# Performance work log

Hardware: AMD Instinct MI355X
Metric: run time of the kernel (lower is better)

The kernel has to match this reference:

```python
import jax, jax.numpy as jnp
import numpy as np

N = 100000      # nodes
E = 1600000     # edges
G = 1024        # graphs in batch
BASE = 1000     # baseline (TF-IDF) dim
AUG = 384       # augmented (LM) dim
H = 256         # hidden dim
C = 2           # classes
EPS = 1e-5      # BatchNorm eps


def setup_inputs() -> dict:
    key = jax.random.key(0)
    ks = jax.random.split(key, 10)
    x = jax.random.normal(ks[0], (N, BASE), jnp.float32)
    x_aug = jax.random.normal(ks[1], (N, AUG), jnp.float32)
    edge_index = jax.random.randint(ks[2], (2, E), 0, N)
    batch = jnp.sort(jax.random.randint(ks[3], (N,), 0, G))

    def lin(k, fin, fout):
        return (jax.random.normal(k, (fin, fout), jnp.float32) / np.sqrt(fin)).astype(jnp.float32)

    return dict(
        x=x, x_aug=x_aug,
        fusion_W=lin(ks[4], BASE + AUG, H), fusion_b=jnp.zeros((H,), jnp.float32),
        W0=lin(ks[5], H, H), b0=jnp.zeros((H,), jnp.float32),
        g0=jnp.ones((H,), jnp.float32), be0=jnp.zeros((H,), jnp.float32),
        W1=lin(ks[6], H, H), b1=jnp.zeros((H,), jnp.float32),
        g1=jnp.ones((H,), jnp.float32), be1=jnp.zeros((H,), jnp.float32),
        fc_W=lin(ks[7], H, C), fc_b=jnp.zeros((C,), jnp.float32),
        edge_index=edge_index, batch=batch,
    )


def _gcn(h, W, b, src, dst, dinv):
    # PyG GCNConv: x' = D^{-1/2}(A+I)D^{-1/2} (x W) + b, self-loop weight 1
    h = h @ W                                     # [N, H]
    norm = dinv[src] * dinv[dst]                  # [E]
    agg = jax.ops.segment_sum(h[src] * norm[:, None], dst, num_segments=N)
    agg = agg + h * (dinv * dinv)[:, None]        # self-loop term
    return agg + b


def _bn(x, gamma, beta):
    # training-mode BatchNorm1d (batch statistics, biased variance)
    m = x.mean(axis=0)
    v = x.var(axis=0)
    return (x - m) * jax.lax.rsqrt(v + EPS) * gamma + beta


def reference(x, x_aug, fusion_W, fusion_b, W0, b0, g0, be0, W1, b1, g1, be1,
              fc_W, fc_b, edge_index, batch):
    src, dst = edge_index[0], edge_index[1]
    # degrees with self-loops (edge weight 1), scattered at destination
    deg = jnp.zeros((N,), x.dtype).at[dst].add(1.0) + 1.0
    dinv = jax.lax.rsqrt(deg)

    # feature fusion ('concat'): Linear(baseline+aug -> hidden) + ReLU
    h = jax.nn.relu(jnp.concatenate([x, x_aug], axis=1) @ fusion_W + fusion_b)

    # GCN layer 1 + BN + ReLU (dropout is identity in eval)
    h = jax.nn.relu(_bn(_gcn(h, W0, b0, src, dst, dinv), g0, be0))
    # GCN layer 2 + BN + ReLU
    h = jax.nn.relu(_bn(_gcn(h, W1, b1, src, dst, dinv), g1, be1))

    # global mean pool over graphs
    cnt = jax.ops.segment_sum(jnp.ones((N,), h.dtype), batch, num_segments=G)
    pooled = jax.ops.segment_sum(h, batch, num_segments=G) / jnp.maximum(cnt, 1.0)[:, None]

    logits = pooled @ fc_W + fc_b                 # [G, C]
    return jax.nn.log_softmax(logits, axis=1)
```

## Files before the change

### kernel.cpp

```cpp
#include <hip/hip_runtime.h>
#include <hip/hip_bf16.h>

#define N_NODES 100000
#define N_EDGES 1600000
#define N_GRAPH 1024
#define DIM_BASE 1000
#define DIM_AUG 384
#define DIM_IN 1384
#define KPAD_IN 1408
#define HD 256
#define BN_EPS 1e-5f

typedef _Float16 f16x8 __attribute__((ext_vector_type(8)));
typedef _Float16 f16x4 __attribute__((ext_vector_type(4)));
typedef float f32x4 __attribute__((ext_vector_type(4)));

__global__ void zero_kernel(unsigned int* __restrict__ p, int n) {
    int i = blockIdx.x * blockDim.x + threadIdx.x;
    if (i < n) p[i] = 0u;
}

__global__ void count_edges_kernel(const int* __restrict__ dst, int* __restrict__ counts, int e) {
    int i = blockIdx.x * blockDim.x + threadIdx.x;
    if (i < e) atomicAdd(&counts[dst[i]], 1);
}

__global__ __launch_bounds__(256) void deg_bsum_kernel(const int* __restrict__ counts,
                                                       int* __restrict__ bsum, int n) {
    __shared__ int sh[256];
    int t = threadIdx.x;
    int base = blockIdx.x * 1024 + t * 4;
    int s = 0;
    if (base < n) {
        int4 v = *(const int4*)&counts[base];
        s = v.x + v.y + v.z + v.w;
    }
    sh[t] = s;
    __syncthreads();
    for (int off = 128; off > 0; off >>= 1) {
        if (t < off) sh[t] += sh[t + off];
        __syncthreads();
    }
    if (t == 0) bsum[blockIdx.x] = sh[0];
}

__global__ __launch_bounds__(128) void scan_bsum_kernel(const int* __restrict__ bsum,
                                                        int* __restrict__ boff, int nb) {
    __shared__ int sh[128];
    int t = threadIdx.x;
    int v = (t < nb) ? bsum[t] : 0;
    sh[t] = v;
    __syncthreads();
    for (int off = 1; off < 128; off <<= 1) {
        int u = (t >= off) ? sh[t - off] : 0;
        __syncthreads();
        sh[t] += u;
        __syncthreads();
    }
    if (t < nb) boff[t] = sh[t] - v;
}

__global__ __launch_bounds__(256) void emit_csr_kernel(const int* __restrict__ counts,
                                                       const int* __restrict__ boff,
                                                       int* __restrict__ row_ptr,
                                                       int* __restrict__ cursor,
                                                       float* __restrict__ dinv, int n, int etot) {
    __shared__ int sh[256];
    int t = threadIdx.x;
    int base = blockIdx.x * 1024 + t * 4;
    int c0 = 0, c1 = 0, c2 = 0, c3 = 0;
    if (base < n) {
        int4 v = *(const int4*)&counts[base];
        c0 = v.x; c1 = v.y; c2 = v.z; c3 = v.w;
    }
    int s = c0 + c1 + c2 + c3;
    sh[t] = s;
    __syncthreads();
    for (int off = 1; off < 256; off <<= 1) {
        int u = (t >= off) ? sh[t - off] : 0;
        __syncthreads();
        sh[t] += u;
        __syncthreads();
    }
    if (base < n) {
        int run = boff[blockIdx.x] + sh[t] - s;
        int4 rp;
        rp.x = run; run += c0;
        rp.y = run; run += c1;
        rp.z = run; run += c2;
        rp.w = run;
        *(int4*)&row_ptr[base] = rp;
        *(int4*)&cursor[base] = rp;
        float4 dv;
        dv.x = rsqrtf((float)c0 + 1.0f);
        dv.y = rsqrtf((float)c1 + 1.0f);
        dv.z = rsqrtf((float)c2 + 1.0f);
        dv.w = rsqrtf((float)c3 + 1.0f);
        *(float4*)&dinv[base] = dv;
    }
    if (blockIdx.x == 0 && t == 0) row_ptr[n] = etot;
}

__global__ void fill_edges_kernel(const int* __restrict__ src, const int* __restrict__ dst,
                                  int* __restrict__ cursor, int* __restrict__ col, int e) {
    int i = blockIdx.x * blockDim.x + threadIdx.x;
    if (i < e) {
        int pos = atomicAdd(&cursor[dst[i]], 1);
        col[pos] = src[i];
    }
}

__global__ __launch_bounds__(256) void btrans_kernel(const float* __restrict__ W,
                                                     f16x8* __restrict__ Bt,
                                                     int K, int nchunks) {
    int idx = blockIdx.x * 256 + threadIdx.x;
    if (idx >= nchunks) return;
    int col = idx & 255;
    int kbase = (idx >> 8) * 8;
    f16x8 h;
#pragma unroll
    for (int j = 0; j < 8; ++j) {
        int k = kbase + j;
        float v = (k < K) ? W[(size_t)k * HD + col] : 0.f;
        h[j] = (_Float16)v;
    }
    Bt[idx] = h;
}

__global__ __launch_bounds__(512, 4) void fusion_mfma_kernel(
        const float* __restrict__ x, const float* __restrict__ xa,
        const f16x8* __restrict__ Bt, const float* __restrict__ bias,
        _Float16* __restrict__ C, int M) {
    __shared__ _Float16 Al[128 * 40];
    __shared__ _Float16 Bl[32 * 256];
    int tid = threadIdx.x;
    int lane = tid & 63;
    int wid = tid >> 6;
    int wr = wid >> 2, wc = wid & 3;
    int l16 = lane & 15, l4 = lane >> 4;
    int row0 = blockIdx.x * 128;

    f32x4 acc[4][4];
#pragma unroll
    for (int m = 0; m < 4; ++m)
#pragma unroll
        for (int n = 0; n < 4; ++n) acc[m][n] = (f32x4){0.f, 0.f, 0.f, 0.f};

    int arow = tid >> 2;
    int akq = (tid & 3) * 8;
    int ar = row0 + arow;

    const int S = KPAD_IN / 32;
    for (int s = 0; s < S; ++s) {
        int kg = s * 32 + akq;
        float fv[8];
#pragma unroll
        for (int j = 0; j < 8; ++j) fv[j] = 0.f;
        if (ar < M && kg < DIM_IN) {
            const float* sp = (kg < DIM_BASE) ? (x + (size_t)ar * DIM_BASE + kg)
                                              : (xa + (size_t)ar * DIM_AUG + (kg - DIM_BASE));
            float4 v0 = ((const float4*)sp)[0];
            float4 v1 = ((const float4*)sp)[1];
            fv[0] = v0.x; fv[1] = v0.y; fv[2] = v0.z; fv[3] = v0.w;
            fv[4] = v1.x; fv[5] = v1.y; fv[6] = v1.z; fv[7] = v1.w;
        }
        f16x8 av;
#pragma unroll
        for (int j = 0; j < 8; ++j) av[j] = (_Float16)fv[j];
        f16x8 bv0 = Bt[(size_t)s * 1024 + tid];
        f16x8 bv1 = Bt[(size_t)s * 1024 + 512 + tid];

        __syncthreads();
        *(f16x8*)&Al[arow * 40 + akq] = av;
        *(f16x8*)&Bl[(size_t)tid * 8] = bv0;
        *(f16x8*)&Bl[(size_t)(512 + tid) * 8] = bv1;
        __syncthreads();

        f16x8 bf[4];
#pragma unroll
        for (int n = 0; n < 4; ++n)
            bf[n] = *(const f16x8*)&Bl[(size_t)(l4 * 256 + wc * 64 + n * 16 + l16) * 8];
#pragma unroll
        for (int m = 0; m < 4; ++m) {
            f16x8 af = *(const f16x8*)&Al[(size_t)(wr * 64 + m * 16 + l16) * 40 + l4 * 8];
#pragma unroll
            for (int n = 0; n < 4; ++n)
                acc[m][n] = __builtin_amdgcn_mfma_f32_16x16x32_f16(af, bf[n], acc[m][n], 0, 0, 0);
        }
    }

#pragma unroll
    for (int n = 0; n < 4; ++n) {
        int colF = wc * 64 + n * 16 + l16;
        float bcol = bias[colF];
#pragma unroll
        for (int m = 0; m < 4; ++m) {
#pragma unroll
            for (int r = 0; r < 4; ++r) {
                int rowF = row0 + wr * 64 + m * 16 + l4 * 4 + r;
                if (rowF < M)
                    C[(size_t)rowF * HD + colF] = (_Float16)fmaxf(acc[m][n][r] + bcol, 0.f);
            }
        }
    }
}

__global__ __launch_bounds__(512, 4) void hgemm_f16_kernel(
        const _Float16* __restrict__ A, const f16x8* __restrict__ Bt,
        _Float16* __restrict__ C, int M) {
    __shared__ _Float16 Al[128 * 40];
    __shared__ _Float16 Bl[32 * 256];
    int tid = threadIdx.x;
    int lane = tid & 63;
    int wid = tid >> 6;
    int wr = wid >> 2, wc = wid & 3;
    int l16 = lane & 15, l4 = lane >> 4;
    int row0 = blockIdx.x * 128;

    f32x4 acc[4][4];
#pragma unroll
    for (int m = 0; m < 4; ++m)
#pragma unroll
        for (int n = 0; n < 4; ++n) acc[m][n] = (f32x4){0.f, 0.f, 0.f, 0.f};

    int arow = tid >> 2;
    int akq = (tid & 3) * 8;
    int ar = row0 + arow;

    const int S = HD / 32;
    for (int s = 0; s < S; ++s) {
        int kg = s * 32 + akq;
        f16x8 av = (f16x8)(_Float16)0;
        if (ar < M) av = *(const f16x8*)&A[(size_t)ar * HD + kg];
        f16x8 bv0 = Bt[(size_t)s * 1024 + tid];
        f16x8 bv1 = Bt[(size_t)s * 1024 + 512 + tid];

        __syncthreads();
        *(f16x8*)&Al[arow * 40 + akq] = av;
        *(f16x8*)&Bl[(size_t)tid * 8] = bv0;
        *(f16x8*)&Bl[(size_t)(512 + tid) * 8] = bv1;
        __syncthreads();

        f16x8 bf[4];
#pragma unroll
        for (int n = 0; n < 4; ++n)
            bf[n] = *(const f16x8*)&Bl[(size_t)(l4 * 256 + wc * 64 + n * 16 + l16) * 8];
#pragma unroll
        for (int m = 0; m < 4; ++m) {
            f16x8 af = *(const f16x8*)&Al[(size_t)(wr * 64 + m * 16 + l16) * 40 + l4 * 8];
#pragma unroll
            for (int n = 0; n < 4; ++n)
                acc[m][n] = __builtin_amdgcn_mfma_f32_16x16x32_f16(af, bf[n], acc[m][n], 0, 0, 0);
        }
    }

#pragma unroll
    for (int n = 0; n < 4; ++n) {
        int colF = wc * 64 + n * 16 + l16;
#pragma unroll
        for (int m = 0; m < 4; ++m) {
#pragma unroll
            for (int r = 0; r < 4; ++r) {
                int rowF = row0 + wr * 64 + m * 16 + l4 * 4 + r;
                if (rowF < M)
                    C[(size_t)rowF * HD + colF] = (_Float16)acc[m][n][r];
            }
        }
    }
}

__global__ __launch_bounds__(512, 4) void hgemm_bn_kernel(
        const float* __restrict__ A, const f16x8* __restrict__ Bt,
        const float* __restrict__ bnp, _Float16* __restrict__ C, int M) {
    __shared__ _Float16 Al[128 * 40];
    __shared__ _Float16 Bl[32 * 256];
    __shared__ float bns[512];
    int tid = threadIdx.x;
    int lane = tid & 63;
    int wid = tid >> 6;
    int wr = wid >> 2, wc = wid & 3;
    int l16 = lane & 15, l4 = lane >> 4;
    int row0 = blockIdx.x * 128;

    bns[tid] = bnp[tid & 511];

    f32x4 acc[4][4];
#pragma unroll
    for (int m = 0; m < 4; ++m)
#pragma unroll
        for (int n = 0; n < 4; ++n) acc[m][n] = (f32x4){0.f, 0.f, 0.f, 0.f};

    int arow = tid >> 2;
    int akq = (tid & 3) * 8;
    int ar = row0 + arow;

    __syncthreads();

    const int S = HD / 32;
    for (int s = 0; s < S; ++s) {
        int kg = s * 32 + akq;
        float fv[8];
#pragma unroll
        for (int j = 0; j < 8; ++j) fv[j] = 0.f;
        if (ar < M) {
            const float* sp = A + (size_t)ar * HD + kg;
            float4 v0 = ((const float4*)sp)[0];
            float4 v1 = ((const float4*)sp)[1];
            fv[0] = v0.x; fv[1] = v0.y; fv[2] = v0.z; fv[3] = v0.w;
            fv[4] = v1.x; fv[5] = v1.y; fv[6] = v1.z; fv[7] = v1.w;
        }
        f16x8 av;
#pragma unroll
        for (int j = 0; j < 8; ++j)
            av[j] = (_Float16)fmaxf(fmaf(fv[j], bns[kg + j], bns[HD + kg + j]), 0.f);
        f16x8 bv0 = Bt[(size_t)s * 1024 + tid];
        f16x8 bv1 = Bt[(size_t)s * 1024 + 512 + tid];

        __syncthreads();
        *(f16x8*)&Al[arow * 40 + akq] = av;
        *(f16x8*)&Bl[(size_t)tid * 8] = bv0;
        *(f16x8*)&Bl[(size_t)(512 + tid) * 8] = bv1;
        __syncthreads();

        f16x8 bf[4];
#pragma unroll
        for (int n = 0; n < 4; ++n)
            bf[n] = *(const f16x8*)&Bl[(size_t)(l4 * 256 + wc * 64 + n * 16 + l16) * 8];
#pragma unroll
        for (int m = 0; m < 4; ++m) {
            f16x8 af = *(const f16x8*)&Al[(size_t)(wr * 64 + m * 16 + l16) * 40 + l4 * 8];
#pragma unroll
            for (int n = 0; n < 4; ++n)
                acc[m][n] = __builtin_amdgcn_mfma_f32_16x16x32_f16(af, bf[n], acc[m][n], 0, 0, 0);
        }
    }

#pragma unroll
    for (int n = 0; n < 4; ++n) {
        int colF = wc * 64 + n * 16 + l16;
#pragma unroll
        for (int m = 0; m < 4; ++m) {
#pragma unroll
            for (int r = 0; r < 4; ++r) {
                int rowF = row0 + wr * 64 + m * 16 + l4 * 4 + r;
                if (rowF < M)
                    C[(size_t)rowF * HD + colF] = (_Float16)acc[m][n][r];
            }
        }
    }
}

__global__ __launch_bounds__(256) void agg_kernel(
        const _Float16* __restrict__ t, const float* __restrict__ dinv,
        const int* __restrict__ row_ptr, const int* __restrict__ col,
        const float* __restrict__ bias, float* __restrict__ outp, int n) {
    int wid = threadIdx.x >> 6;
    int lane = threadIdx.x & 63;
    int i = blockIdx.x * 4 + wid;
    if (i >= n) return;
    int c0 = lane * 4;
    float di = dinv[i];
    float di2 = di * di;
    f16x4 sv = *(const f16x4*)&t[(size_t)i * HD + c0];
    float a0 = (float)sv[0] * di2, a1 = (float)sv[1] * di2;
    float a2 = (float)sv[2] * di2, a3 = (float)sv[3] * di2;
    int e = row_ptr[i], end = row_ptr[i + 1];
    for (; e + 1 < end; e += 2) {
        int s0 = col[e], s1 = col[e + 1];
        float w0 = dinv[s0] * di, w1 = dinv[s1] * di;
        f16x4 v0 = *(const f16x4*)&t[(size_t)s0 * HD + c0];
        f16x4 v1 = *(const f16x4*)&t[(size_t)s1 * HD + c0];
        a0 = fmaf((float)v0[0], w0, a0); a1 = fmaf((float)v0[1], w0, a1);
        a2 = fmaf((float)v0[2], w0, a2); a3 = fmaf((float)v0[3], w0, a3);
        a0 = fmaf((float)v1[0], w1, a0); a1 = fmaf((float)v1[1], w1, a1);
        a2 = fmaf((float)v1[2], w1, a2); a3 = fmaf((float)v1[3], w1, a3);
    }
    if (e < end) {
        int s0 = col[e];
        float w0 = dinv[s0] * di;
        f16x4 v0 = *(const f16x4*)&t[(size_t)s0 * HD + c0];
        a0 = fmaf((float)v0[0], w0, a0); a1 = fmaf((float)v0[1], w0, a1);
        a2 = fmaf((float)v0[2], w0, a2); a3 = fmaf((float)v0[3], w0, a3);
    }
    float4 b = *(const float4*)&bias[c0];
    float4 o;
    o.x = a0 + b.x; o.y = a1 + b.y; o.z = a2 + b.z; o.w = a3 + b.w;
    *(float4*)&outp[(size_t)i * HD + c0] = o;
}

__global__ __launch_bounds__(256) void bn_stats_kernel(const float* __restrict__ a,
                                                       float* __restrict__ sums, int n) {
    int tid = threadIdx.x;
    int r0 = blockIdx.x * 256;
    int r1 = min(r0 + 256, n);
    float s = 0.f, s2 = 0.f;
    for (int r = r0; r < r1; ++r) {
        float v = a[(size_t)r * HD + tid];
        s += v;
        s2 = fmaf(v, v, s2);
    }
    atomicAdd(&sums[tid], s);
    atomicAdd(&sums[HD + tid], s2);
}

__global__ __launch_bounds__(256) void bn_final_kernel(const float* __restrict__ sums,
                                                       const float* __restrict__ g,
                                                       const float* __restrict__ be,
                                                       float* __restrict__ p, int n) {
    int tid = threadIdx.x;
    float mean = sums[tid] / (float)n;
    float var = sums[HD + tid] / (float)n - mean * mean;
    float sc = g[tid] * rsqrtf(var + BN_EPS);
    p[tid] = sc;
    p[HD + tid] = be[tid] - mean * sc;
}

__global__ void graph_cnt_kernel(const int* __restrict__ batch, float* __restrict__ cnt, int n) {
    int i = blockIdx.x * blockDim.x + threadIdx.x;
    if (i < n) atomicAdd(&cnt[batch[i]], 1.0f);
}

__global__ __launch_bounds__(256) void bn_relu_pool_kernel(const float* __restrict__ a,
                                                           const float* __restrict__ p,
                                                           const int* __restrict__ batch,
                                                           float* __restrict__ pooled, int n) {
    int tid = threadIdx.x;
    int n0 = blockIdx.x * 64;
    int n1 = min(n0 + 64, n);
    if (n0 >= n) return;
    float sc = p[tid], sh = p[HD + tid];
    int curg = batch[n0];
    float acc = 0.f;
    for (int i = n0; i < n1; ++i) {
        int g = batch[i];
        if (g != curg) {
            atomicAdd(&pooled[(size_t)curg * HD + tid], acc);
            acc = 0.f;
            curg = g;
        }
        acc += fmaxf(fmaf(a[(size_t)i * HD + tid], sc, sh), 0.f);
    }
    atomicAdd(&pooled[(size_t)curg * HD + tid], acc);
}

__global__ __launch_bounds__(64) void head_kernel(const float* __restrict__ pooled,
                                                  const float* __restrict__ cnt,
                                                  const float* __restrict__ fcW,
                                                  const float* __restrict__ fcb,
                                                  float* __restrict__ outp) {
    int g = blockIdx.x, lane = threadIdx.x;
    float inv = 1.0f / fmaxf(cnt[g], 1.0f);
    float a0 = 0.f, a1 = 0.f;
    for (int j = lane; j < HD; j += 64) {
        float v = pooled[(size_t)g * HD + j] * inv;
        a0 = fmaf(v, fcW[j * 2 + 0], a0);
        a1 = fmaf(v, fcW[j * 2 + 1], a1);
    }
    for (int off = 32; off > 0; off >>= 1) {
        a0 += __shfl_down(a0, off);
        a1 += __shfl_down(a1, off);
    }
    if (lane == 0) {
        float l0 = a0 + fcb[0], l1 = a1 + fcb[1];
        float m = fmaxf(l0, l1);
        float lse = m + logf(expf(l0 - m) + expf(l1 - m));
        outp[g * 2 + 0] = l0 - lse;
        outp[g * 2 + 1] = l1 - lse;
    }
}

extern "C" void kernel_launch(void* const* d_in, const int* in_sizes, int n_in,
                              void* d_out, int out_size, void* d_ws, size_t ws_size,
                              hipStream_t stream) {
    const float* x        = (const float*)d_in[0];
    const float* x_aug    = (const float*)d_in[1];
    const float* fusion_W = (const float*)d_in[2];
    const float* fusion_b = (const float*)d_in[3];
    const float* W0       = (const float*)d_in[4];
    const float* b0       = (const float*)d_in[5];
    const float* g0       = (const float*)d_in[6];
    const float* be0      = (const float*)d_in[7];
    const float* W1       = (const float*)d_in[8];
    const float* b1       = (const float*)d_in[9];
    const float* g1       = (const float*)d_in[10];
    const float* be1      = (const float*)d_in[11];
    const float* fc_W     = (const float*)d_in[12];
    const float* fc_b     = (const float*)d_in[13];
    const int*   eidx     = (const int*)d_in[14];
    const int*   batch    = (const int*)d_in[15];
    float* outp = (float*)d_out;

    const int N = N_NODES, E = N_EDGES, G = N_GRAPH;
    const int* src = eidx;
    const int* dst = eidx + E;

    size_t off = 0;
    char* ws = (char*)d_ws;
    auto take = [&](size_t nbytes) -> void* {
        void* p = ws + off;
        off = (off + nbytes + 255) & ~(size_t)255;
        return p;
    };
    float*     bufA    = (float*)take((size_t)N * HD * 4);
    _Float16*  bufH    = (_Float16*)take((size_t)N * HD * 2);
    _Float16*  bufT    = (_Float16*)take((size_t)N * HD * 2);
    float*     dinv    = (float*)take((size_t)N * 4);
    int*       row_ptr = (int*)take((size_t)(N + 1) * 4);
    int*       cursor  = (int*)take((size_t)N * 4);
    int*       col     = (int*)take((size_t)E * 4);
    float*     bn1p    = (float*)take(512 * 4);
    float*     bn2p    = (float*)take(512 * 4);
    int*       bsum    = (int*)take(128 * 4);
    int*       boff    = (int*)take(128 * 4);
    f16x8*     BtF     = (f16x8*)take((size_t)(KPAD_IN / 8) * 256 * 16);
    f16x8*     Bt0     = (f16x8*)take((size_t)(HD / 8) * 256 * 16);
    f16x8*     Bt1     = (f16x8*)take((size_t)(HD / 8) * 256 * 16);
    size_t zwords = (size_t)N + 512 + 512 + (size_t)G * HD + G;
    unsigned int* zbase = (unsigned int*)take(zwords * 4);
    int*   counts = (int*)zbase;
    float* bn1s   = (float*)(zbase + N);
    float* bn2s   = bn1s + 512;
    float* pooled = bn2s + 512;
    float* cnt    = pooled + (size_t)G * HD;

    const int nchF = (KPAD_IN / 8) * 256;
    const int nchH = (HD / 8) * 256;
    const int nScanB = (N + 1023) / 1024;

    zero_kernel<<<(int)((zwords + 255) / 256), 256, 0, stream>>>(zbase, (int)zwords);
    count_edges_kernel<<<(E + 255) / 256, 256, 0, stream>>>(dst, counts, E);
    deg_bsum_kernel<<<nScanB, 256, 0, stream>>>(counts, bsum, N);
    scan_bsum_kernel<<<1, 128, 0, stream>>>(bsum, boff, nScanB);
    emit_csr_kernel<<<nScanB, 256, 0, stream>>>(counts, boff, row_ptr, cursor, dinv, N, E);
    fill_edges_kernel<<<(E + 255) / 256, 256, 0, stream>>>(src, dst, cursor, col, E);
    btrans_kernel<<<(nchF + 255) / 256, 256, 0, stream>>>(fusion_W, BtF, DIM_IN, nchF);
    btrans_kernel<<<(nchH + 255) / 256, 256, 0, stream>>>(W0, Bt0, HD, nchH);
    btrans_kernel<<<(nchH + 255) / 256, 256, 0, stream>>>(W1, Bt1, HD, nchH);

    const int gblocks = (N + 127) / 128;
    fusion_mfma_kernel<<<gblocks, 512, 0, stream>>>(x, x_aug, BtF, fusion_b, bufH, N);
    hgemm_f16_kernel<<<gblocks, 512, 0, stream>>>(bufH, Bt0, bufT, N);
    agg_kernel<<<(N + 3) / 4, 256, 0, stream>>>(bufT, dinv, row_ptr, col, b0, bufA, N);
    bn_stats_kernel<<<(N + 255) / 256, 256, 0, stream>>>(bufA, bn1s, N);
    bn_final_kernel<<<1, 256, 0, stream>>>(bn1s, g0, be0, bn1p, N);
    hgemm_bn_kernel<<<gblocks, 512, 0, stream>>>(bufA, Bt1, bn1p, bufT, N);
    agg_kernel<<<(N + 3) / 4, 256, 0, stream>>>(bufT, dinv, row_ptr, col, b1, bufA, N);
    bn_stats_kernel<<<(N + 255) / 256, 256, 0, stream>>>(bufA, bn2s, N);
    bn_final_kernel<<<1, 256, 0, stream>>>(bn2s, g1, be1, bn2p, N);
    graph_cnt_kernel<<<(N + 255) / 256, 256, 0, stream>>>(batch, cnt, N);
    bn_relu_pool_kernel<<<(N + 63) / 64, 256, 0, stream>>>(bufA, bn2p, batch, pooled, N);
    head_kernel<<<G, 64, 0, stream>>>(pooled, cnt, fc_W, fc_b, outp);
}
```

Measured before the change: 1.002 ms.

## Double-buffer A tiles in LDS, prefetch A two steps ahead, read B from global

All three GEMM kernels now double-buffer the A tile in shared memory with one barrier per k-step instead of two. A-tile global loads are issued two steps ahead into registers so they overlap the MFMA work. The B operand no longer goes through LDS; each wave reads its B fragments straight from global memory (likely L2/L1 hits) into registers. Out-of-range rows are clamped instead of branched on. This cuts barrier and LDS traffic at the cost of more global B reads and register pressure.

```diff
diff --git a/kernel.cpp b/kernel.cpp
--- a/kernel.cpp
+++ b/kernel.cpp
@@ -131,8 +131,7 @@
         const float* __restrict__ x, const float* __restrict__ xa,
         const f16x8* __restrict__ Bt, const float* __restrict__ bias,
         _Float16* __restrict__ C, int M) {
-    __shared__ _Float16 Al[128 * 40];
-    __shared__ _Float16 Bl[32 * 256];
+    __shared__ _Float16 Al[2][128 * 40];
     int tid = threadIdx.x;
     int lane = tid & 63;
     int wid = tid >> 6;
@@ -149,57 +148,67 @@
     int arow = tid >> 2;
     int akq = (tid & 3) * 8;
     int ar = row0 + arow;
-
-    const int S = KPAD_IN / 32;
-    for (int s = 0; s < S; ++s) {
+    int arc = (ar < M) ? ar : (M - 1);
+
+    auto loadA = [&](int s, float* fv) {
         int kg = s * 32 + akq;
-        float fv[8];
-#pragma unroll
-        for (int j = 0; j < 8; ++j) fv[j] = 0.f;
-        if (ar < M && kg < DIM_IN) {
-            const float* sp = (kg < DIM_BASE) ? (x + (size_t)ar * DIM_BASE + kg)
-                                              : (xa + (size_t)ar * DIM_AUG + (kg - DIM_BASE));
+        if (kg < DIM_IN) {
+            const float* sp = (kg < DIM_BASE) ? (x + (size_t)arc * DIM_BASE + kg)
+                                              : (xa + (size_t)arc * DIM_AUG + (kg - DIM_BASE));
             float4 v0 = ((const float4*)sp)[0];
             float4 v1 = ((const float4*)sp)[1];
             fv[0] = v0.x; fv[1] = v0.y; fv[2] = v0.z; fv[3] = v0.w;
             fv[4] = v1.x; fv[5] = v1.y; fv[6] = v1.z; fv[7] = v1.w;
-        }
+        } else {
+#pragma unroll
+            for (int j = 0; j < 8; ++j) fv[j] = 0.f;
+        }
+    };
+
+    const int S = KPAD_IN / 32;
+    float fv0[8], fv1[8];
+    loadA(0, fv0);
+    loadA(1, fv1);
+
+    int bcol = wc * 64 + l16;
+
+    auto iter = [&](int s, float* fv) {
+        int buf = s & 1;
         f16x8 av;
 #pragma unroll
         for (int j = 0; j < 8; ++j) av[j] = (_Float16)fv[j];
-        f16x8 bv0 = Bt[(size_t)s * 1024 + tid];
-        f16x8 bv1 = Bt[(size_t)s * 1024 + 512 + tid];
-
-        __syncthreads();
-        *(f16x8*)&Al[arow * 40 + akq] = av;
-        *(f16x8*)&Bl[(size_t)tid * 8] = bv0;
-        *(f16x8*)&Bl[(size_t)(512 + tid) * 8] = bv1;
-        __syncthreads();
-
+        *(f16x8*)&Al[buf][arow * 40 + akq] = av;
+        if (s + 2 < S) loadA(s + 2, fv);
+        __syncthreads();
         f16x8 bf[4];
 #pragma unroll
         for (int n = 0; n < 4; ++n)
-            bf[n] = *(const f16x8*)&Bl[(size_t)(l4 * 256 + wc * 64 + n * 16 + l16) * 8];
+            bf[n] = Bt[(size_t)(s * 4 + l4) * 256 + bcol + n * 16];
 #pragma unroll
         for (int m = 0; m < 4; ++m) {
-            f16x8 af = *(const f16x8*)&Al[(size_t)(wr * 64 + m * 16 + l16) * 40 + l4 * 8];
+            f16x8 af = *(const f16x8*)&Al[buf][(wr * 64 + m * 16 + l16) * 40 + l4 * 8];
 #pragma unroll
             for (int n = 0; n < 4; ++n)
                 acc[m][n] = __builtin_amdgcn_mfma_f32_16x16x32_f16(af, bf[n], acc[m][n], 0, 0, 0);
         }
+    };
+
+    for (int s = 0; s < S; s += 2) {
+        iter(s, fv0);
+        iter(s + 1, fv1);
     }
 
 #pragma unroll
     for (int n = 0; n < 4; ++n) {
         int colF = wc * 64 + n * 16 + l16;
-        float bcol = bias[colF];
+        float bc = bias[colF];
 #pragma unroll
         for (int m = 0; m < 4; ++m) {
 #pragma unroll
             for (int r = 0; r < 4; ++r) {
                 int rowF = row0 + wr * 64 + m * 16 + l4 * 4 + r;
                 if (rowF < M)
-                    C[(size_t)rowF * HD + colF] = (_Float16)fmaxf(acc[m][n][r] + bcol, 0.f);
+                    C[(size_t)rowF * HD + colF] = (_Float16)fmaxf(acc[m][n][r] + bc, 0.f);
             }
         }
     }
@@ -208,8 +217,7 @@
 __global__ __launch_bounds__(512, 4) void hgemm_f16_kernel(
         const _Float16* __restrict__ A, const f16x8* __restrict__ Bt,
         _Float16* __restrict__ C, int M) {
-    __shared__ _Float16 Al[128 * 40];
-    __shared__ _Float16 Bl[32 * 256];
+    __shared__ _Float16 Al[2][128 * 40];
     int tid = threadIdx.x;
     int lane = tid & 63;
     int wid = tid >> 6;
@@ -226,32 +234,34 @@
     int arow = tid >> 2;
     int akq = (tid & 3) * 8;
     int ar = row0 + arow;
+    int arc = (ar < M) ? ar : (M - 1);
+    int bcol = wc * 64 + l16;
 
     const int S = HD / 32;
-    for (int s = 0; s < S; ++s) {
-        int kg = s * 32 + akq;
-        f16x8 av = (f16x8)(_Float16)0;
-        if (ar < M) av = *(const f16x8*)&A[(size_t)ar * HD + kg];
-        f16x8 bv0 = Bt[(size_t)s * 1024 + tid];
-        f16x8 bv1 = Bt[(size_t)s * 1024 + 512 + tid];
-
-        __syncthreads();
-        *(f16x8*)&Al[arow * 40 + akq] = av;
-        *(f16x8*)&Bl[(size_t)tid * 8] = bv0;
-        *(f16x8*)&Bl[(size_t)(512 + tid) * 8] = bv1;
-        __syncthreads();
-
+    f16x8 av0 = *(const f16x8*)&A[(size_t)arc * HD + akq];
+    f16x8 av1 = *(const f16x8*)&A[(size_t)arc * HD + 32 + akq];
+
+    auto iter = [&](int s, f16x8& av) {
+        int buf = s & 1;
+        *(f16x8*)&Al[buf][arow * 40 + akq] = av;
+        if (s + 2 < S) av = *(const f16x8*)&A[(size_t)arc * HD + (s + 2) * 32 + akq];
+        __syncthreads();
         f16x8 bf[4];
 #pragma unroll
         for (int n = 0; n < 4; ++n)
-            bf[n] = *(const f16x8*)&Bl[(size_t)(l4 * 256 + wc * 64 + n * 16 + l16) * 8];
+            bf[n] = Bt[(size_t)(s * 4 + l4) * 256 + bcol + n * 16];
 #pragma unroll
         for (int m = 0; m < 4; ++m) {
-            f16x8 af = *(const f16x8*)&Al[(size_t)(wr * 64 + m * 16 + l16) * 40 + l4 * 8];
+            f16x8 af = *(const f16x8*)&Al[buf][(wr * 64 + m * 16 + l16) * 40 + l4 * 8];
 #pragma unroll
             for (int n = 0; n < 4; ++n)
                 acc[m][n] = __builtin_amdgcn_mfma_f32_16x16x32_f16(af, bf[n], acc[m][n], 0, 0, 0);
         }
+    };
+
+    for (int s = 0; s < S; s += 2) {
+        iter(s, av0);
+        iter(s + 1, av1);
     }
 
 #pragma unroll
@@ -272,8 +282,7 @@
 __global__ __launch_bounds__(512, 4) void hgemm_bn_kernel(
         const float* __restrict__ A, const f16x8* __restrict__ Bt,
         const float* __restrict__ bnp, _Float16* __restrict__ C, int M) {
-    __shared__ _Float16 Al[128 * 40];
-    __shared__ _Float16 Bl[32 * 256];
+    __shared__ _Float16 Al[2][128 * 40];
     __shared__ float bns[512];
     int tid = threadIdx.x;
     int lane = tid & 63;
@@ -282,7 +291,8 @@
     int l16 = lane & 15, l4 = lane >> 4;
     int row0 = blockIdx.x * 128;
 
-    bns[tid] = bnp[tid & 511];
+    bns[tid] = bnp[tid];
+    __syncthreads();
 
     f32x4 acc[4][4];
 #pragma unroll
@@ -293,46 +303,48 @@
     int arow = tid >> 2;
     int akq = (tid & 3) * 8;
     int ar = row0 + arow;
-
-    __syncthreads();
+    int arc = (ar < M) ? ar : (M - 1);
+    int bcol = wc * 64 + l16;
+
+    auto loadA = [&](int s, float* fv) {
+        const float* sp = A + (size_t)arc * HD + s * 32 + akq;
+        float4 v0 = ((const float4*)sp)[0];
+        float4 v1 = ((const float4*)sp)[1];
+        fv[0] = v0.x; fv[1] = v0.y; fv[2] = v0.z; fv[3] = v0.w;
+        fv[4] = v1.x; fv[5] = v1.y; fv[6] = v1.z; fv[7] = v1.w;
+    };
 
     const int S = HD / 32;
-    for (int s = 0; s < S; ++s) {
+    float fv0[8], fv1[8];
+    loadA(0, fv0);
+    loadA(1, fv1);
+
+    auto iter = [&](int s, float* fv) {
+        int buf = s & 1;
         int kg = s * 32 + akq;
-        float fv[8];
-#pragma unroll
-        for (int j = 0; j < 8; ++j) fv[j] = 0.f;
-        if (ar < M) {
-            const float* sp = A + (size_t)ar * HD + kg;
-            float4 v0 = ((const float4*)sp)[0];
-            float4 v1 = ((const float4*)sp)[1];
-            fv[0] = v0.x; fv[1] = v0.y; fv[2] = v0.z; fv[3] = v0.w;
-            fv[4] = v1.x; fv[5] = v1.y; fv[6] = v1.z; fv[7] = v1.w;
-        }
         f16x8 av;
 #pragma unroll
         for (int j = 0; j < 8; ++j)
             av[j] = (_Float16)fmaxf(fmaf(fv[j], bns[kg + j], bns[HD + kg + j]), 0.f);
-        f16x8 bv0 = Bt[(size_t)s * 1024 + tid];
-        f16x8 bv1 = Bt[(size_t)s * 1024 + 512 + tid];
-
-        __syncthreads();
-        *(f16x8*)&Al[arow * 40 + akq] = av;
-        *(f16x8*)&Bl[(size_t)tid * 8] = bv0;
-        *(f16x8*)&Bl[(size_t)(512 + tid) * 8] = bv1;
-        __syncthreads();
-
+        *(f16x8*)&Al[buf][arow * 40 + akq] = av;
+        if (s + 2 < S) loadA(s + 2, fv);
+        __syncthreads();
         f16x8 bf[4];
 #pragma unroll
         for (int n = 0; n < 4; ++n)
-            bf[n] = *(const f16x8*)&Bl[(size_t)(l4 * 256 + wc * 64 + n * 16 + l16) * 8];
+            bf[n] = Bt[(size_t)(s * 4 + l4) * 256 + bcol + n * 16];
 #pragma unroll
         for (int m = 0; m < 4; ++m) {
-            f16x8 af = *(const f16x8*)&Al[(size_t)(wr * 64 + m * 16 + l16) * 40 + l4 * 8];
+            f16x8 af = *(const f16x8*)&Al[buf][(wr * 64 + m * 16 + l16) * 40 + l4 * 8];
 #pragma unroll
             for (int n = 0; n < 4; ++n)
                 acc[m][n] = __builtin_amdgcn_mfma_f32_16x16x32_f16(af, bf[n], acc[m][n], 0, 0, 0);
         }
+    };
+
+    for (int s = 0; s < S; s += 2) {
+        iter(s, fv0);
+        iter(s + 1, fv1);
     }
 
 #pragma unroll
```

Result: no change. 1.017 ms (+1.5%).
